# Performance work log

Hardware: AMD Instinct MI355X
Metric: run time of the kernel (lower is better)

Reference implementation:

```python
import jax, jax.numpy as jnp
import numpy as np

N_FEATURES = 3072
LATENT_DIM = 128
BATCH = 8192


def setup_inputs() -> dict:
    key = jax.random.key(0)
    k1, k2, k3, k4 = jax.random.split(key, 4)
    example = jax.random.normal(k1, (BATCH, N_FEATURES), dtype=jnp.float32)
    # small-ish W so C = W W^T + sigma^2 I is well conditioned
    W = jax.random.normal(k2, (N_FEATURES, LATENT_DIM), dtype=jnp.float32) * 0.05
    log_var = jax.random.normal(k3, (1,), dtype=jnp.float32) * 0.1
    training_mean = jax.random.normal(k4, (N_FEATURES,), dtype=jnp.float32)
    return {"example": example, "W": W, "log_var": log_var, "training_mean": training_mean}


def reference(example, W, log_var, training_mean):
    n = W.shape[0]
    # C = W W^T + exp(log_var) * I   -- [n, n] covariance, as in the original
    C = W @ W.T + jnp.exp(log_var[0]) * jnp.eye(n, dtype=W.dtype)
    _, logdetC = jnp.linalg.slogdet(C)
    precision = jnp.linalg.inv(C)
    res = example.reshape(-1, n) - training_mean.reshape(1, n)  # [B, n]
    # diag(res @ precision @ res^T) computed directly, avoiding the BxB matrix
    quad = jnp.einsum("bi,ij,bj->b", res, precision, res)  # [B]
    log_2pi = np.log(2.0 * np.pi).astype(np.float32)
    log_like = -0.5 * (n * log_2pi + logdetC + quad)  # [B]
    return log_like
```

## Files before the change

### kernel.cpp

```cpp
#include <hip/hip_runtime.h>
#include <hip/hip_bf16.h>

#define N_FEAT 3072
#define LATENT 128
#define LOG2PI 1.8378770664093453f

typedef __attribute__((ext_vector_type(8))) short short8;
typedef __attribute__((ext_vector_type(4))) float f32x4;

__device__ __forceinline__ unsigned short f2bf(float x) {
  unsigned int u = __float_as_uint(x);
  u += 0x7FFFu + ((u >> 16) & 1u);
  return (unsigned short)(u >> 16);
}

typedef __attribute__((address_space(1))) const void gas_void;
typedef __attribute__((address_space(3))) void las_void;
__device__ __forceinline__ void gld_lds16(const void* g, void* s) {
  __builtin_amdgcn_global_load_lds((gas_void*)g, (las_void*)s, 16, 0, 0);
}

__global__ __launch_bounds__(256) void k_prep(const float* __restrict__ W,
                                              float* __restrict__ Mp,
                                              unsigned short* __restrict__ Wt) {
  __shared__ __align__(16) float Ws[64 * 128];
  int t = threadIdx.x;
  int k0 = blockIdx.x * 64;
  const float* src = W + (size_t)k0 * 128;
#pragma unroll
  for (int c = 0; c < 8; ++c)
    ((float4*)Ws)[t + 256 * c] = ((const float4*)src)[t + 256 * c];
  __syncthreads();
  int tr = t >> 4, tc = t & 15;
  float acc[8][8];
#pragma unroll
  for (int r = 0; r < 8; ++r)
#pragma unroll
    for (int c = 0; c < 8; ++c) acc[r][c] = 0.f;
#pragma unroll 2
  for (int k = 0; k < 64; ++k) {
    f32x4 a0 = *(f32x4*)&Ws[k * 128 + 8 * tr];
    f32x4 a1 = *(f32x4*)&Ws[k * 128 + 8 * tr + 4];
    f32x4 b0 = *(f32x4*)&Ws[k * 128 + 8 * tc];
    f32x4 b1 = *(f32x4*)&Ws[k * 128 + 8 * tc + 4];
    float av[8] = {a0.x, a0.y, a0.z, a0.w, a1.x, a1.y, a1.z, a1.w};
    float bv[8] = {b0.x, b0.y, b0.z, b0.w, b1.x, b1.y, b1.z, b1.w};
#pragma unroll
    for (int r = 0; r < 8; ++r)
#pragma unroll
      for (int c = 0; c < 8; ++c) acc[r][c] = fmaf(av[r], bv[c], acc[r][c]);
  }
  float* dst = Mp + (size_t)blockIdx.x * 16384 + (size_t)(8 * tr) * 128 + 8 * tc;
#pragma unroll
  for (int r = 0; r < 8; ++r) {
    *(f32x4*)(dst + r * 128) = (f32x4){acc[r][0], acc[r][1], acc[r][2], acc[r][3]};
    *(f32x4*)(dst + r * 128 + 4) = (f32x4){acc[r][4], acc[r][5], acc[r][6], acc[r][7]};
  }
  int n = t >> 1, h = t & 1;
  unsigned pk[16];
#pragma unroll
  for (int c = 0; c < 16; ++c)
    pk[c] = (unsigned)f2bf(Ws[(h * 32 + 2 * c) * 128 + n]) |
            ((unsigned)f2bf(Ws[(h * 32 + 2 * c + 1) * 128 + n]) << 16);
  uint4* wd = (uint4*)(Wt + (size_t)n * N_FEAT + k0 + h * 32);
#pragma unroll
  for (int c = 0; c < 4; ++c)
    wd[c] = make_uint4(pk[4 * c], pk[4 * c + 1], pk[4 * c + 2], pk[4 * c + 3]);
}

__global__ __launch_bounds__(256) void k_red(const float* __restrict__ Mp,
                                             float* __restrict__ M) {
  int i = blockIdx.x * 256 + threadIdx.x;
  float s = 0.f;
#pragma unroll
  for (int p = 0; p < 48; ++p) s += Mp[(size_t)p * 16384 + i];
  M[i] = s;
}

__device__ __forceinline__ void inverse_body(char* smem, int t, float* M,
                                             float* scal,
                                             const float* log_var) {
  float* sh = (float*)smem;
  float* PR = sh;
  float* PC = sh + 256;
  float* DB = sh + 512;
  float* DG = sh + 514;
  float* RD = sh + 642;
  bool act = t < 256;
  int itr = t >> 4, itc = t & 15;
  float lv = log_var[0];
  float sig2 = expf(lv);
  float a[8][8];
  if (act) {
    const float* srcM = M + (size_t)(8 * itr) * 128 + 8 * itc;
#pragma unroll
    for (int r = 0; r < 8; ++r) {
      f32x4 v0 = *(const f32x4*)(srcM + r * 128);
      f32x4 v1 = *(const f32x4*)(srcM + r * 128 + 4);
      a[r][0] = v0.x; a[r][1] = v0.y; a[r][2] = v0.z; a[r][3] = v0.w;
      a[r][4] = v1.x; a[r][5] = v1.y; a[r][6] = v1.z; a[r][7] = v1.w;
    }
    if (itr == itc) {
#pragma unroll
      for (int r = 0; r < 8; ++r) a[r][r] += sig2;
    }
    if (itr == 0) {
#pragma unroll
      for (int c = 0; c < 8; ++c) PR[8 * itc + c] = a[0][c];
    }
    if (itc == 0) {
#pragma unroll
      for (int r = 0; r < 8; ++r) PC[8 * itr + r] = a[r][0];
    }
    if (t == 0) DB[0] = a[0][0];
  }
  __syncthreads();
  for (int kb = 0; kb < 16; ++kb) {
#pragma unroll
    for (int lk = 0; lk < 8; ++lk) {
      const int k = kb * 8 + lk;
      const int buf = k & 1;
      if (act) {
        float d = DB[buf];
        if (t == 0) DG[k] = d;
        float p = 1.0f / d;
        float pr[8], pc[8];
#pragma unroll
        for (int c = 0; c < 8; ++c) pr[c] = PR[buf * 128 + 8 * itc + c] * p;
#pragma unroll
        for (int r = 0; r < 8; ++r) pc[r] = PC[buf * 128 + 8 * itr + r];
#pragma unroll
        for (int r = 0; r < 8; ++r)
#pragma unroll
          for (int c = 0; c < 8; ++c) a[r][c] = fmaf(-pc[r], pr[c], a[r][c]);
        bool myrow = (itr == (k >> 3));
        bool mycol = (itc == (k >> 3));
        if (myrow) {
#pragma unroll
          for (int c = 0; c < 8; ++c) a[lk][c] = pr[c];
        }
        if (mycol) {
#pragma unroll
          for (int r = 0; r < 8; ++r) a[r][lk] = -p * pc[r];
        }
        if (myrow && mycol) a[lk][lk] = p;
        if (k + 1 < 128) {
          const int nb = buf ^ 1;
          const int nl = (lk + 1) & 7;
          const int nr = (k + 1) >> 3;
          if (itr == nr) {
#pragma unroll
            for (int c = 0; c < 8; ++c) PR[nb * 128 + 8 * itc + c] = a[nl][c];
          }
          if (itc == nr) {
#pragma unroll
            for (int r = 0; r < 8; ++r) PC[nb * 128 + 8 * itr + r] = a[r][nl];
          }
          if (itr == nr && itc == nr) DB[nb] = a[nl][nl];
        }
      }
      __syncthreads();
    }
  }
  if (act) {
    float* dst = M + (size_t)(8 * itr) * 128 + 8 * itc;
#pragma unroll
    for (int r = 0; r < 8; ++r) {
      f32x4 v0 = {a[r][0], a[r][1], a[r][2], a[r][3]};
      f32x4 v1 = {a[r][4], a[r][5], a[r][6], a[r][7]};
      *(f32x4*)(dst + r * 128) = v0;
      *(f32x4*)(dst + r * 128 + 4) = v1;
    }
  }
  float ld = 0.f;
  if (t < 128) ld = logf(DG[t]);
#pragma unroll
  for (int o = 1; o < 64; o <<= 1) ld += __shfl_xor(ld, o);
  if (t == 0) RD[0] = ld;
  if (t == 64) RD[1] = ld;
  __syncthreads();
  if (t == 0) {
    scal[0] = -0.5f * (N_FEAT * LOG2PI + (float)(N_FEAT - LATENT) * lv +
                       (RD[0] + RD[1]));
    scal[1] = expf(-lv);
  }
}

__device__ __forceinline__ void gemm_body(char* smem, int rg, int half, int t,
                                          const float* ex, const float* mean,
                                          const unsigned short* Wt, float* Tp,
                                          float* sqp) {
  char* As = smem;
  char* Bs = smem + 16384;
  int r0 = rg * 32;
  int tg0 = half * 12;
  int lane = t & 63, w = t >> 6;

  int arow = t >> 4, ag = t & 15;
  const float* ep = ex + (size_t)(r0 + arow) * N_FEAT + (size_t)tg0 * 128 + ag * 8;
  const float* mp = mean + (size_t)tg0 * 128 + ag * 8;
  int awoff = arow * 256 + ((ag & 8) + ((ag + arow) & 7)) * 16;

  int sp = lane & 15, rl = lane >> 4;
  const unsigned short* bsrc[4];
#pragma unroll
  for (int j = 0; j < 4; ++j) {
    int n = w * 16 + j * 4 + rl;
    int s = (sp & 8) | ((sp - n) & 7);
    bsrc[j] = Wt + (size_t)n * N_FEAT + (size_t)tg0 * 128 + s * 8;
  }
  char* ldsB0 = Bs + (size_t)w * 4096;
  char* ldsB1 = Bs + 32768 + (size_t)w * 4096;

  int fr = lane & 15, fq = lane >> 4;
  int aoff0[4], aoff1[4], boff[4];
#pragma unroll
  for (int kk = 0; kk < 4; ++kk) {
    int sI = kk * 4 + fq;
    aoff0[kk] = fr * 256 + ((sI & 8) + ((sI + fr) & 7)) * 16;
    int ar1 = 16 + fr;
    aoff1[kk] = ar1 * 256 + ((sI & 8) + ((sI + ar1) & 7)) * 16;
    int n = w * 16 + fr;
    boff[kk] = n * 256 + ((sI & 8) + ((sI + n) & 7)) * 16;
  }

  f32x4 acc0 = {0.f, 0.f, 0.f, 0.f}, acc1 = {0.f, 0.f, 0.f, 0.f};
  float sq = 0.f;
  float4 eA, eA2, mA, mA2;
  float4 eB, eB2, mB, mB2;

  auto loadS0 = [&](int it) {
    const float* p = ep + (size_t)it * 128;
    const float* q = mp + (size_t)it * 128;
    eA = *(const float4*)p;  eA2 = *(const float4*)(p + 4);
    mA = *(const float4*)q;  mA2 = *(const float4*)(q + 4);
  };
  auto loadS1 = [&](int it) {
    const float* p = ep + (size_t)it * 128;
    const float* q = mp + (size_t)it * 128;
    eB = *(const float4*)p;  eB2 = *(const float4*)(p + 4);
    mB = *(const float4*)q;  mB2 = *(const float4*)(q + 4);
  };
  auto packS = [&](const float4& e, const float4& e2, const float4& m,
                   const float4& m2, int bufN) {
    float r0_ = e.x - m.x,   r1_ = e.y - m.y,   r2_ = e.z - m.z,   r3_ = e.w - m.w;
    float r4_ = e2.x - m2.x, r5_ = e2.y - m2.y, r6_ = e2.z - m2.z, r7_ = e2.w - m2.w;
    sq = fmaf(r0_, r0_, sq); sq = fmaf(r1_, r1_, sq);
    sq = fmaf(r2_, r2_, sq); sq = fmaf(r3_, r3_, sq);
    sq = fmaf(r4_, r4_, sq); sq = fmaf(r5_, r5_, sq);
    sq = fmaf(r6_, r6_, sq); sq = fmaf(r7_, r7_, sq);
    uint4 pa;
    pa.x = (unsigned)f2bf(r0_) | ((unsigned)f2bf(r1_) << 16);
    pa.y = (unsigned)f2bf(r2_) | ((unsigned)f2bf(r3_) << 16);
    pa.z = (unsigned)f2bf(r4_) | ((unsigned)f2bf(r5_) << 16);
    pa.w = (unsigned)f2bf(r6_) | ((unsigned)f2bf(r7_) << 16);
    *(uint4*)(As + bufN * 8192 + awoff) = pa;
  };
  auto issueB = [&](int it, int bufN) {
    char* d = bufN ? ldsB1 : ldsB0;
#pragma unroll
    for (int j = 0; j < 4; ++j)
      gld_lds16(bsrc[j] + (size_t)it * 128, d + j * 1024);
  };
  auto mma = [&](int bufN) {
    char* Ab = As + bufN * 8192;
    char* Bb = Bs + bufN * 32768;
#pragma unroll
    for (int kk = 0; kk < 4; ++kk) {
      short8 a0 = *(const short8*)(Ab + aoff0[kk]);
      short8 a1 = *(const short8*)(Ab + aoff1[kk]);
      short8 b  = *(const short8*)(Bb + boff[kk]);
      acc0 = __builtin_amdgcn_mfma_f32_16x16x32_bf16(a0, b, acc0, 0, 0, 0);
      acc1 = __builtin_amdgcn_mfma_f32_16x16x32_bf16(a1, b, acc1, 0, 0, 0);
    }
  };

  loadS0(0);
  loadS1(1);
  __builtin_amdgcn_sched_barrier(0);
  issueB(0, 0);
  packS(eA, eA2, mA, mA2, 0);
  loadS0(2);
  asm volatile("s_waitcnt lgkmcnt(0)" ::: "memory");
  __builtin_amdgcn_s_barrier();
  __builtin_amdgcn_sched_barrier(0);

#pragma unroll
  for (int j = 0; j < 5; ++j) {
    const int it0 = 2 * j;
    issueB(it0 + 1, 1);
    asm volatile("s_waitcnt vmcnt(8)" ::: "memory");
    __builtin_amdgcn_sched_barrier(0);
    mma(0);
    packS(eB, eB2, mB, mB2, 1);
    loadS1(it0 + 3 < 12 ? it0 + 3 : 11);
    asm volatile("s_waitcnt lgkmcnt(0)" ::: "memory");
    __builtin_amdgcn_s_barrier();
    __builtin_amdgcn_sched_barrier(0);
    issueB(it0 + 2, 0);
    asm volatile("s_waitcnt vmcnt(8)" ::: "memory");
    __builtin_amdgcn_sched_barrier(0);
    mma(1);
    packS(eA, eA2, mA, mA2, 0);
    loadS0(it0 + 4 < 12 ? it0 + 4 : 11);
    asm volatile("s_waitcnt lgkmcnt(0)" ::: "memory");
    __builtin_amdgcn_s_barrier();
    __builtin_amdgcn_sched_barrier(0);
  }
  issueB(11, 1);
  asm volatile("s_waitcnt vmcnt(8)" ::: "memory");
  __builtin_amdgcn_sched_barrier(0);
  mma(0);
  packS(eB, eB2, mB, mB2, 1);
  asm volatile("s_waitcnt lgkmcnt(0)" ::: "memory");
  __builtin_amdgcn_s_barrier();
  __builtin_amdgcn_sched_barrier(0);
  asm volatile("s_waitcnt vmcnt(0)" ::: "memory");
  __builtin_amdgcn_sched_barrier(0);
  mma(1);

  sq += __shfl_xor(sq, 1); sq += __shfl_xor(sq, 2);
  sq += __shfl_xor(sq, 4); sq += __shfl_xor(sq, 8);
  if (ag == 0) sqp[half * 8192 + r0 + arow] = sq;

  float* tp = Tp + (size_t)half * 1048576 +
              (size_t)(r0 + fq * 4) * 128 + w * 16 + fr;
#pragma unroll
  for (int ii = 0; ii < 4; ++ii) {
    tp[(size_t)ii * 128] = acc0[ii];
    tp[(size_t)ii * 128 + 2048] = acc1[ii];
  }
}

__global__ __launch_bounds__(512, 4) void k_gemm(
    const float* __restrict__ ex, const float* __restrict__ mean,
    const unsigned short* __restrict__ Wt, float* __restrict__ M,
    float* __restrict__ scal, const float* __restrict__ lv,
    float* __restrict__ Tp, float* __restrict__ sqp) {
  __shared__ __align__(16) char smem[81920];
  int bid = blockIdx.x, t = threadIdx.x;
  int rg, half;
  if (bid == 0) {
    inverse_body(smem, t, M, scal, lv);
    __syncthreads();
    rg = 255; half = 1;
  } else {
    int g = bid - 1;
    rg = g & 255; half = g >> 8;
  }
  gemm_body(smem, rg, half, t, ex, mean, Wt, Tp, sqp);
}

__global__ __launch_bounds__(256) void k_epi(const float* __restrict__ Tp,
                                             const float* __restrict__ sqp,
                                             const float* __restrict__ Minv,
                                             const float* __restrict__ scal,
                                             float* __restrict__ out) {
  __shared__ __align__(16) float Ts[32][132];
  __shared__ float rs[32];
  int t = threadIdx.x;
  int r0 = blockIdx.x * 32;
  int sr = t >> 3, sseg = t & 7;
  const float* tp0 = Tp + (size_t)(r0 + sr) * 128 + sseg * 16;
  const float* tp1 = tp0 + 1048576;
#pragma unroll
  for (int c = 0; c < 4; ++c) {
    float4 v0 = *(const float4*)(tp0 + c * 4);
    float4 v1 = *(const float4*)(tp1 + c * 4);
    *(f32x4*)&Ts[sr][sseg * 16 + c * 4] =
        (f32x4){v0.x + v1.x, v0.y + v1.y, v0.z + v1.z, v0.w + v1.w};
  }
  if (t < 32) rs[t] = sqp[r0 + t] + sqp[8192 + r0 + t];
  __syncthreads();

  int rp = t >> 4, cg2 = t & 15;
  int ra = 2 * rp, rb = ra + 1;
  int c0 = cg2 * 8;
  float ya[8] = {0, 0, 0, 0, 0, 0, 0, 0};
  float yb[8] = {0, 0, 0, 0, 0, 0, 0, 0};
#pragma unroll 4
  for (int j = 0; j < 128; ++j) {
    float tav = Ts[ra][j];
    float tbv = Ts[rb][j];
    float4 v0 = *(const float4*)(Minv + j * LATENT + c0);
    float4 v1 = *(const float4*)(Minv + j * LATENT + c0 + 4);
    ya[0] = fmaf(tav, v0.x, ya[0]); ya[1] = fmaf(tav, v0.y, ya[1]);
    ya[2] = fmaf(tav, v0.z, ya[2]); ya[3] = fmaf(tav, v0.w, ya[3]);
    ya[4] = fmaf(tav, v1.x, ya[4]); ya[5] = fmaf(tav, v1.y, ya[5]);
    ya[6] = fmaf(tav, v1.z, ya[6]); ya[7] = fmaf(tav, v1.w, ya[7]);
    yb[0] = fmaf(tbv, v0.x, yb[0]); yb[1] = fmaf(tbv, v0.y, yb[1]);
    yb[2] = fmaf(tbv, v0.z, yb[2]); yb[3] = fmaf(tbv, v0.w, yb[3]);
    yb[4] = fmaf(tbv, v1.x, yb[4]); yb[5] = fmaf(tbv, v1.y, yb[5]);
    yb[6] = fmaf(tbv, v1.z, yb[6]); yb[7] = fmaf(tbv, v1.w, yb[7]);
  }
  float q0 = 0.f, q1 = 0.f;
#pragma unroll
  for (int c = 0; c < 8; ++c) {
    q0 = fmaf(ya[c], Ts[ra][c0 + c], q0);
    q1 = fmaf(yb[c], Ts[rb][c0 + c], q1);
  }
  q0 += __shfl_xor(q0, 1); q0 += __shfl_xor(q0, 2);
  q0 += __shfl_xor(q0, 4); q0 += __shfl_xor(q0, 8);
  q1 += __shfl_xor(q1, 1); q1 += __shfl_xor(q1, 2);
  q1 += __shfl_xor(q1, 4); q1 += __shfl_xor(q1, 8);
  if (cg2 == 0) {
    float cc = scal[0], is2 = scal[1];
    out[r0 + ra] = cc - 0.5f * is2 * (rs[ra] - q0);
    out[r0 + rb] = cc - 0.5f * is2 * (rs[rb] - q1);
  }
}

extern "C" void kernel_launch(void* const* d_in, const int* in_sizes, int n_in,
                              void* d_out, int out_size, void* d_ws, size_t ws_size,
                              hipStream_t stream) {
  (void)in_sizes; (void)n_in; (void)out_size; (void)ws_size;
  const float* ex   = (const float*)d_in[0];
  const float* W    = (const float*)d_in[1];
  const float* lv   = (const float*)d_in[2];
  const float* mean = (const float*)d_in[3];
  float* out = (float*)d_out;

  float* M = (float*)d_ws;
  float* scal = M + 16384;
  float* Tp = scal + 64;
  float* sqp = Tp + 2097152;
  unsigned short* Wt = (unsigned short*)(sqp + 16384);
  float* Mp = Tp;

  k_prep<<<48, 256, 0, stream>>>(W, Mp, Wt);
  k_red<<<64, 256, 0, stream>>>(Mp, M);
  k_gemm<<<512, 512, 0, stream>>>(ex, mean, Wt, M, scal, lv, Tp, sqp);
  k_epi<<<256, 256, 0, stream>>>(Tp, sqp, M, scal, out);
}
```

Before: 226.1 us.

## Single-buffer B tiles in GEMM and give inverse its own high-priority block

The GEMM main loop now keeps only one LDS buffer for the W^T tiles. Each wave re-fills its own B slice right after its MFMAs finish, and the A residual tiles stay double-buffered. This cuts shared memory from 80KB to 48KB and raises the launch-bounds occupancy hint. Block 0 now only computes the inverse, at raised wave priority, and no longer also runs the last GEMM tile, with one extra block added to the grid. The intent is to take the serial inverse-then-GEMM chain off the critical path and allow more resident blocks. The cost is less latency hiding for B loads, and inverse_body must now fit in the smaller shared buffer.

```diff
diff --git a/kernel.cpp b/kernel.cpp
--- a/kernel.cpp
+++ b/kernel.cpp
@@ -209,8 +209,7 @@
     int s = (sp & 8) | ((sp - n) & 7);
     bsrc[j] = Wt + (size_t)n * N_FEAT + (size_t)tg0 * 128 + s * 8;
   }
-  char* ldsB0 = Bs + (size_t)w * 4096;
-  char* ldsB1 = Bs + 32768 + (size_t)w * 4096;
+  char* ldsB = Bs + (size_t)w * 4096;
 
   int fr = lane & 15, fq = lane >> 4;
   int aoff0[4], aoff1[4], boff[4];
@@ -226,23 +225,15 @@
 
   f32x4 acc0 = {0.f, 0.f, 0.f, 0.f}, acc1 = {0.f, 0.f, 0.f, 0.f};
   float sq = 0.f;
-  float4 eA, eA2, mA, mA2;
-  float4 eB, eB2, mB, mB2;
-
-  auto loadS0 = [&](int it) {
+  float4 e, e2, m, m2;
+
+  auto loadA = [&](int it) {
     const float* p = ep + (size_t)it * 128;
     const float* q = mp + (size_t)it * 128;
-    eA = *(const float4*)p;  eA2 = *(const float4*)(p + 4);
-    mA = *(const float4*)q;  mA2 = *(const float4*)(q + 4);
+    e  = *(const float4*)p;  e2 = *(const float4*)(p + 4);
+    m  = *(const float4*)q;  m2 = *(const float4*)(q + 4);
   };
-  auto loadS1 = [&](int it) {
-    const float* p = ep + (size_t)it * 128;
-    const float* q = mp + (size_t)it * 128;
-    eB = *(const float4*)p;  eB2 = *(const float4*)(p + 4);
-    mB = *(const float4*)q;  mB2 = *(const float4*)(q + 4);
-  };
-  auto packS = [&](const float4& e, const float4& e2, const float4& m,
-                   const float4& m2, int bufN) {
+  auto packA = [&](int bufN) {
     float r0_ = e.x - m.x,   r1_ = e.y - m.y,   r2_ = e.z - m.z,   r3_ = e.w - m.w;
     float r4_ = e2.x - m2.x, r5_ = e2.y - m2.y, r6_ = e2.z - m2.z, r7_ = e2.w - m2.w;
     sq = fmaf(r0_, r0_, sq); sq = fmaf(r1_, r1_, sq);
@@ -256,67 +247,47 @@
     pa.w = (unsigned)f2bf(r6_) | ((unsigned)f2bf(r7_) << 16);
     *(uint4*)(As + bufN * 8192 + awoff) = pa;
   };
-  auto issueB = [&](int it, int bufN) {
-    char* d = bufN ? ldsB1 : ldsB0;
+  auto issueB = [&](int it) {
 #pragma unroll
     for (int j = 0; j < 4; ++j)
-      gld_lds16(bsrc[j] + (size_t)it * 128, d + j * 1024);
+      gld_lds16(bsrc[j] + (size_t)it * 128, ldsB + j * 1024);
   };
-  auto mma = [&](int bufN) {
-    char* Ab = As + bufN * 8192;
-    char* Bb = Bs + bufN * 32768;
+  auto mma = [&](int bufA) {
+    char* Ab = As + bufA * 8192;
 #pragma unroll
     for (int kk = 0; kk < 4; ++kk) {
       short8 a0 = *(const short8*)(Ab + aoff0[kk]);
       short8 a1 = *(const short8*)(Ab + aoff1[kk]);
-      short8 b  = *(const short8*)(Bb + boff[kk]);
+      short8 b  = *(const short8*)(Bs + boff[kk]);
       acc0 = __builtin_amdgcn_mfma_f32_16x16x32_bf16(a0, b, acc0, 0, 0, 0);
       acc1 = __builtin_amdgcn_mfma_f32_16x16x32_bf16(a1, b, acc1, 0, 0, 0);
     }
   };
 
-  loadS0(0);
-  loadS1(1);
+  loadA(0);
+  packA(0);
   __builtin_amdgcn_sched_barrier(0);
-  issueB(0, 0);
-  packS(eA, eA2, mA, mA2, 0);
-  loadS0(2);
+  issueB(0);
+  loadA(1);
   asm volatile("s_waitcnt lgkmcnt(0)" ::: "memory");
   __builtin_amdgcn_s_barrier();
+  asm volatile("s_waitcnt vmcnt(4)" ::: "memory");
   __builtin_amdgcn_sched_barrier(0);
 
 #pragma unroll
-  for (int j = 0; j < 5; ++j) {
-    const int it0 = 2 * j;
-    issueB(it0 + 1, 1);
-    asm volatile("s_waitcnt vmcnt(8)" ::: "memory");
+  for (int it = 0; it < 11; ++it) {
+    mma(it & 1);
+    asm volatile("s_waitcnt lgkmcnt(0)" ::: "memory");
     __builtin_amdgcn_sched_barrier(0);
-    mma(0);
-    packS(eB, eB2, mB, mB2, 1);
-    loadS1(it0 + 3 < 12 ? it0 + 3 : 11);
+    issueB(it + 1);
+    __builtin_amdgcn_sched_barrier(0);
+    packA((it + 1) & 1);
+    loadA(it + 2 <= 11 ? it + 2 : 11);
     asm volatile("s_waitcnt lgkmcnt(0)" ::: "memory");
     __builtin_amdgcn_s_barrier();
+    asm volatile("s_waitcnt vmcnt(4)" ::: "memory");
     __builtin_amdgcn_sched_barrier(0);
-    issueB(it0 + 2, 0);
-    asm volatile("s_waitcnt vmcnt(8)" ::: "memory");
-    __builtin_amdgcn_sched_barrier(0);
-    mma(1);
-    packS(eA, eA2, mA, mA2, 0);
-    loadS0(it0 + 4 < 12 ? it0 + 4 : 11);
-    asm volatile("s_waitcnt lgkmcnt(0)" ::: "memory");
-    __builtin_amdgcn_s_barrier();
-    __builtin_amdgcn_sched_barrier(0);
-  }
-  issueB(11, 1);
-  asm volatile("s_waitcnt vmcnt(8)" ::: "memory");
-  __builtin_amdgcn_sched_barrier(0);
-  mma(0);
-  packS(eB, eB2, mB, mB2, 1);
-  asm volatile("s_waitcnt lgkmcnt(0)" ::: "memory");
-  __builtin_amdgcn_s_barrier();
-  __builtin_amdgcn_sched_barrier(0);
-  asm volatile("s_waitcnt vmcnt(0)" ::: "memory");
-  __builtin_amdgcn_sched_barrier(0);
+  }
   mma(1);
 
   sq += __shfl_xor(sq, 1); sq += __shfl_xor(sq, 2);
@@ -332,23 +303,21 @@
   }
 }
 
-__global__ __launch_bounds__(512, 4) void k_gemm(
+__global__ __launch_bounds__(512, 6) void k_gemm(
     const float* __restrict__ ex, const float* __restrict__ mean,
     const unsigned short* __restrict__ Wt, float* __restrict__ M,
     float* __restrict__ scal, const float* __restrict__ lv,
     float* __restrict__ Tp, float* __restrict__ sqp) {
-  __shared__ __align__(16) char smem[81920];
+  __shared__ __align__(16) char smem[49152];
   int bid = blockIdx.x, t = threadIdx.x;
-  int rg, half;
   if (bid == 0) {
+    __builtin_amdgcn_s_setprio(1);
     inverse_body(smem, t, M, scal, lv);
-    __syncthreads();
-    rg = 255; half = 1;
-  } else {
-    int g = bid - 1;
-    rg = g & 255; half = g >> 8;
-  }
-  gemm_body(smem, rg, half, t, ex, mean, Wt, Tp, sqp);
+    __builtin_amdgcn_s_setprio(0);
+    return;
+  }
+  int g = bid - 1;
+  gemm_body(smem, g & 255, g >> 8, t, ex, mean, Wt, Tp, sqp);
 }
 
 __global__ __launch_bounds__(256) void k_epi(const float* __restrict__ Tp,
@@ -429,6 +398,6 @@
 
   k_prep<<<48, 256, 0, stream>>>(W, Mp, Wt);
   k_red<<<64, 256, 0, stream>>>(Mp, M);
-  k_gemm<<<512, 512, 0, stream>>>(ex, mean, Wt, M, scal, lv, Tp, sqp);
+  k_gemm<<<513, 512, 0, stream>>>(ex, mean, Wt, M, scal, lv, Tp, sqp);
   k_epi<<<256, 256, 0, stream>>>(Tp, sqp, M, scal, out);
 }
```

Result: slower. 725.5 us (+220.8%).
